# Optimization experiments

Measured on AMD Instinct MI355X. Metric: run time of the kernel, lower is better.

The kernel has to match this reference:

```python
import jax, jax.numpy as jnp
import numpy as np

TOL = 0.0
MARGIN = 0.0
REVERSE = False
SIZE_AVERAGE = True

N, C, H, W = 128, 256, 32, 64


def setup_inputs() -> dict:
    key = jax.random.key(0)
    k1, k2 = jax.random.split(key)
    raw_feat = jax.random.normal(k1, (N, C, H, W), dtype=jnp.float32)
    rectified_feat = jax.random.normal(k2, (N, C, H, W), dtype=jnp.float32)
    return {"raw_feat": raw_feat, "rectified_feat": rectified_feat}


def _rank(feat):
    # feat: [n, c, h, w] -> channel mean -> [n, h, w]
    n, c, h, w = feat.shape
    m = jnp.mean(feat, axis=1)                       # [n, h, w]
    flat = m.reshape(n, -1)
    nrm = jnp.linalg.norm(flat, axis=1, keepdims=True)
    normed = (flat / nrm).reshape(n, h, w)
    # batched singular values of small h x w matrices
    s = jnp.linalg.svd(normed, compute_uv=False)     # [n, min(h,w)]
    return jnp.sum((s > TOL).astype(jnp.float32), axis=1)  # [n]


def reference(raw_feat, rectified_feat):
    rank1 = _rank(raw_feat)
    rank2 = _rank(rectified_feat)
    y = jnp.full_like(rank1, -1.0 if REVERSE else 1.0)
    # margin ranking loss: max(0, -y*(x1-x2)+margin), no per-element reduction
    loss = jnp.maximum(0.0, -y * (rank1 - rank2) + MARGIN)
    if SIZE_AVERAGE:
        loss = jnp.sum(loss) / raw_feat.shape[0]
    return loss
```

## Files before the change

### kernel.cpp

```cpp
#include <hip/hip_runtime.h>
#include <math.h>


#define N_BATCH 128
#define C_CH    256
#define H_DIM   32
#define W_DIM   64
#define HW      (H_DIM * W_DIM)
#define HW4     (HW / 4)

__global__ __launch_bounds__(256) void channel_sum_kernel(
    const float* __restrict__ raw, const float* __restrict__ rect,
    float* __restrict__ m )
{
    int v = blockIdx.x * blockDim.x + threadIdx.x;
    int input = v >> 16;
    int rem   = v & 0xFFFF;
    int n     = rem >> 9;
    int hw4   = rem & 511;

    const float4* src = (const float4*)(input ? rect : raw);
    const float4* p = src + (size_t)(n * C_CH) * HW4 + hw4;

    float4 acc = make_float4(0.f, 0.f, 0.f, 0.f);
#pragma unroll 4
    for (int c = 0; c < C_CH; ++c) {
        float4 x = p[(size_t)c * HW4];
        acc.x += x.x; acc.y += x.y; acc.z += x.z; acc.w += x.w;
    }
    float4* dst = (float4*)m;
    dst[(size_t)v] = acc;
}

__global__ __launch_bounds__(64) void rank_kernel(
    const float* __restrict__ m, float* __restrict__ ranks)
{
    __shared__ float A[H_DIM][W_DIM + 1];
    __shared__ float f[H_DIM];
    __shared__ int   s_piv;

    int mat = blockIdx.x;
    int t   = threadIdx.x;
    const float* src = m + (size_t)mat * HW;

    for (int i = 0; i < H_DIM; ++i) A[i][t] = src[i * W_DIM + t];
    __syncthreads();

    int r = 0;
    for (int c = 0; c < W_DIM && r < H_DIM; ++c) {
        if (t == 0) {
            int p = r; float best = fabsf(A[r][c]);
            for (int i = r + 1; i < H_DIM; ++i) {
                float av = fabsf(A[i][c]);
                if (av > best) { best = av; p = i; }
            }
            s_piv = (best > 0.0f) ? p : -1;
        }
        __syncthreads();
        int p = s_piv;
        if (p >= 0) {
            if (p != r) {
                float tmp = A[r][t]; A[r][t] = A[p][t]; A[p][t] = tmp;
            }
            __syncthreads();
            if (t > r && t < H_DIM) f[t] = A[t][c] / A[r][c];
            __syncthreads();
            if (t >= c) {
                float arj = A[r][t];
                for (int i = r + 1; i < H_DIM; ++i) A[i][t] -= f[i] * arj;
            }
            ++r;
        }
        __syncthreads();
    }
    if (t == 0) ranks[mat] = (float)r;
}

__global__ __launch_bounds__(128) void loss_kernel(
    const float* __restrict__ ranks, float* __restrict__ out)
{
    __shared__ float red[128];
    int t = threadIdx.x;
    float r1 = ranks[t];
    float r2 = ranks[N_BATCH + t];
    red[t] = fmaxf(0.0f, -(r1 - r2));
    __syncthreads();
    for (int s = 64; s > 0; s >>= 1) {
        if (t < s) red[t] += red[t + s];
        __syncthreads();
    }
    if (t == 0) out[0] = red[0] / (float)N_BATCH;
}

extern "C" void kernel_launch(void* const* d_in, const int* in_sizes, int n_in,
                              void* d_out, int out_size, void* d_ws, size_t ws_size,
                              hipStream_t stream)
{
    const float* raw  = (const float*)d_in[0];
    const float* rect = (const float*)d_in[1];
    float* out = (float*)d_out;

    float* m     = (float*)d_ws;
    float* ranks = m + 2 * N_BATCH * HW;

    channel_sum_kernel<<<131072 / 256, 256, 0, stream>>>(raw, rect, m);
    rank_kernel<<<2 * N_BATCH, 64, 0, stream>>>(m, ranks);
    loss_kernel<<<1, 128, 0, stream>>>(ranks, out);
}
```

Measured before the change: 152.7 us.

## Split channel reduction across chunks and move rank elimination into registers

The channel-mean sum is split into four channel chunks written to partial buffers and combined by a second small kernel, raising the thread count for the memory-bound read. The rank kernel replaces shared-memory Gaussian elimination with per-thread register columns, using wave shuffles and a used-row bitmask for pivoting, which removes the many block barriers. This costs an extra partial-buffer write/read and more register pressure, and the split path depends on sufficient workspace.

```diff
diff --git a/kernel.cpp b/kernel.cpp
--- a/kernel.cpp
+++ b/kernel.cpp
@@ -8,72 +8,91 @@
 #define W_DIM   64
 #define HW      (H_DIM * W_DIM)
 #define HW4     (HW / 4)
+#define PLANE4  (2 * N_BATCH * HW4)
 
-__global__ __launch_bounds__(256) void channel_sum_kernel(
+template <int KCT>
+__global__ __launch_bounds__(256) void channel_sum_part(
     const float* __restrict__ raw, const float* __restrict__ rect,
-    float* __restrict__ m )
+    float* __restrict__ part)
 {
     int v = blockIdx.x * blockDim.x + threadIdx.x;
-    int input = v >> 16;
-    int rem   = v & 0xFFFF;
-    int n     = rem >> 9;
-    int hw4   = rem & 511;
+    int k    = v >> 17;
+    int rem  = v & (PLANE4 - 1);
+    int input = rem >> 16;
+    int rem2  = rem & 0xFFFF;
+    int n     = rem2 >> 9;
+    int hw4   = rem2 & 511;
 
+    const int CPK = C_CH / KCT;
     const float4* src = (const float4*)(input ? rect : raw);
-    const float4* p = src + (size_t)(n * C_CH) * HW4 + hw4;
+    const float4* p = src + ((size_t)n * C_CH + (size_t)k * CPK) * HW4 + hw4;
 
     float4 acc = make_float4(0.f, 0.f, 0.f, 0.f);
-#pragma unroll 4
-    for (int c = 0; c < C_CH; ++c) {
+#pragma unroll 8
+    for (int c = 0; c < CPK; ++c) {
         float4 x = p[(size_t)c * HW4];
         acc.x += x.x; acc.y += x.y; acc.z += x.z; acc.w += x.w;
     }
-    float4* dst = (float4*)m;
-    dst[(size_t)v] = acc;
+    ((float4*)part)[(size_t)v] = acc;
+}
+
+template <int KCT>
+__global__ __launch_bounds__(256) void channel_sum_reduce(float* __restrict__ part)
+{
+    int v = blockIdx.x * blockDim.x + threadIdx.x;
+    float4* p = (float4*)part;
+    float4 a = p[v];
+#pragma unroll
+    for (int k = 1; k < KCT; ++k) {
+        float4 x = p[(size_t)k * PLANE4 + v];
+        a.x += x.x; a.y += x.y; a.z += x.z; a.w += x.w;
+    }
+    p[v] = a;
 }
 
 __global__ __launch_bounds__(64) void rank_kernel(
     const float* __restrict__ m, float* __restrict__ ranks)
 {
-    __shared__ float A[H_DIM][W_DIM + 1];
-    __shared__ float f[H_DIM];
-    __shared__ int   s_piv;
-
     int mat = blockIdx.x;
     int t   = threadIdx.x;
     const float* src = m + (size_t)mat * HW;
 
-    for (int i = 0; i < H_DIM; ++i) A[i][t] = src[i * W_DIM + t];
-    __syncthreads();
+    float a[H_DIM];
+#pragma unroll
+    for (int i = 0; i < H_DIM; ++i) a[i] = src[i * W_DIM + t];
 
-    int r = 0;
-    for (int c = 0; c < W_DIM && r < H_DIM; ++c) {
-        if (t == 0) {
-            int p = r; float best = fabsf(A[r][c]);
-            for (int i = r + 1; i < H_DIM; ++i) {
-                float av = fabsf(A[i][c]);
-                if (av > best) { best = av; p = i; }
+    unsigned used = 0;
+    int rank = 0;
+    for (int c = 0; c < W_DIM; ++c) {
+        float v[H_DIM];
+#pragma unroll
+        for (int i = 0; i < H_DIM; ++i) v[i] = __shfl(a[i], c);
+
+        float best = 0.0f; int p = -1;
+#pragma unroll
+        for (int i = 0; i < H_DIM; ++i) {
+            float av = fabsf(v[i]);
+            bool cand = (((used >> i) & 1u) == 0u) && (av > best);
+            best = cand ? av : best;
+            p    = cand ? i  : p;
+        }
+        if (p >= 0) {
+            used |= (1u << p);
+            ++rank;
+            float ap = 0.0f, vp = 1.0f;
+#pragma unroll
+            for (int i = 0; i < H_DIM; ++i) {
+                if (i == p) { ap = a[i]; vp = v[i]; }
             }
-            s_piv = (best > 0.0f) ? p : -1;
+            float inv = 1.0f / vp;
+#pragma unroll
+            for (int i = 0; i < H_DIM; ++i) {
+                if (((used >> i) & 1u) == 0u) a[i] -= (v[i] * inv) * ap;
+            }
+            if (rank == H_DIM) break;
         }
-        __syncthreads();
-        int p = s_piv;
-        if (p >= 0) {
-            if (p != r) {
-                float tmp = A[r][t]; A[r][t] = A[p][t]; A[p][t] = tmp;
-            }
-            __syncthreads();
-            if (t > r && t < H_DIM) f[t] = A[t][c] / A[r][c];
-            __syncthreads();
-            if (t >= c) {
-                float arj = A[r][t];
-                for (int i = r + 1; i < H_DIM; ++i) A[i][t] -= f[i] * arj;
-            }
-            ++r;
-        }
-        __syncthreads();
     }
-    if (t == 0) ranks[mat] = (float)r;
+    if (t == 0) ranks[mat] = (float)rank;
 }
 
 __global__ __launch_bounds__(128) void loss_kernel(
@@ -100,10 +119,19 @@
     const float* rect = (const float*)d_in[1];
     float* out = (float*)d_out;
 
-    float* m     = (float*)d_ws;
-    float* ranks = m + 2 * N_BATCH * HW;
+    float* part = (float*)d_ws;
 
-    channel_sum_kernel<<<131072 / 256, 256, 0, stream>>>(raw, rect, m);
-    rank_kernel<<<2 * N_BATCH, 64, 0, stream>>>(m, ranks);
-    loss_kernel<<<1, 128, 0, stream>>>(ranks, out);
+    const size_t need4 = (size_t)4 * PLANE4 * 4 * sizeof(float) + 1024;
+    if (ws_size >= need4) {
+        float* ranks = part + (size_t)4 * PLANE4 * 4;
+        channel_sum_part<4><<<(PLANE4 * 4) / 256, 256, 0, stream>>>(raw, rect, part);
+        channel_sum_reduce<4><<<PLANE4 / 256, 256, 0, stream>>>(part);
+        rank_kernel<<<2 * N_BATCH, 64, 0, stream>>>(part, ranks);
+        loss_kernel<<<1, 128, 0, stream>>>(ranks, out);
+    } else {
+        float* ranks = part + (size_t)PLANE4 * 4;
+        channel_sum_part<1><<<PLANE4 / 256, 256, 0, stream>>>(raw, rect, part);
+        rank_kernel<<<2 * N_BATCH, 64, 0, stream>>>(part, ranks);
+        loss_kernel<<<1, 128, 0, stream>>>(ranks, out);
+    }
 }
```

Result: faster. 145.0 us (-5.1%).
